# Optimization experiments

Measured on AMD Instinct MI355X. Metric: run time of the kernel, lower is better.

Reference implementation:

```python
import jax, jax.numpy as jnp
import numpy as np

N_TOKENS = 8192
D_MODEL = 1024
N_EXPERTS = 8
TOP_K = 2


def setup_inputs() -> dict:
    key = jax.random.key(0)
    ks = jax.random.split(key, 4)
    scale = 1.0 / np.sqrt(D_MODEL)
    x = jax.random.normal(ks[0], (N_TOKENS, D_MODEL), dtype=jnp.float32)
    gate_w = jax.random.uniform(ks[1], (N_EXPERTS, D_MODEL), jnp.float32, -scale, scale)
    expert_w = jax.random.uniform(ks[2], (N_EXPERTS, D_MODEL, D_MODEL), jnp.float32, -scale, scale)
    expert_b = jax.random.uniform(ks[3], (N_EXPERTS, D_MODEL), jnp.float32, -scale, scale)
    return {"x": x, "gate_w": gate_w, "expert_w": expert_w, "expert_b": expert_b}


def reference(x, gate_w, expert_w, expert_b):
    # Router: logits [N, E], softmax in fp32, top-k, renormalize over selected.
    router_logits = jnp.einsum('nd,ed->ne', x, gate_w)
    probs = jax.nn.softmax(router_logits.astype(jnp.float32), axis=1)
    rw, sel = jax.lax.top_k(probs, TOP_K)            # [N, K]
    rw = rw / jnp.sum(rw, axis=-1, keepdims=True)

    # Dense combine weights [N, E]: routing weight for selected experts, 0 else.
    n_idx = jnp.arange(x.shape[0])[:, None]
    w_dense = jnp.zeros((x.shape[0], N_EXPERTS), jnp.float32).at[n_idx, sel].set(rw)

    # Compute all experts for all tokens (vectorized equivalent of the
    # gather -> Linear -> weighted scatter-add loop; zero weight for
    # unselected experts reproduces the sparse dispatch exactly).
    # expert_w[e] is torch nn.Linear weight [out, in]: y = x @ W^T + b
    h = jnp.einsum('nd,ehd->neh', x, expert_w) + expert_b[None, :, :]  # [N, E, H]
    final = jnp.einsum('neh,ne->nh', h, w_dense.astype(x.dtype))
    return final, router_logits
```

## Files before the change

kernel.cpp:

```cpp
#include <hip/hip_runtime.h>
#include <hip/hip_bf16.h>
#include <stdint.h>

#define NT 8192
#define DM 1024
#define NE 8
#define MAX_TILES 160
#define SLOTS_MAX 17408
#define NKT (DM / 64)

typedef __bf16 bf16x8 __attribute__((ext_vector_type(8)));
typedef float f32x4 __attribute__((ext_vector_type(4)));

typedef const __attribute__((address_space(1))) void* gp_t;
typedef __attribute__((address_space(3))) void* lp_t;
#define GLDS(g, l) __builtin_amdgcn_global_load_lds((gp_t)(g), (lp_t)(l), 16, 0, 0)

__device__ inline unsigned short f2bf(float f) {
  unsigned int u = __float_as_uint(f);
  unsigned int r = (u + 0x7fffu + ((u >> 16) & 1u)) >> 16;
  return (unsigned short)r;
}
__device__ inline float bf2f(unsigned short u) {
  return __uint_as_float((unsigned int)u << 16);
}

__global__ void router_kernel(const float* __restrict__ x,
                              const float* __restrict__ gw,
                              float* __restrict__ logits,
                              unsigned short* __restrict__ xb,
                              int* __restrict__ top2e,
                              float* __restrict__ top2w) {
  const int n = blockIdx.x;
  const int lane = threadIdx.x;
  const float* xr = x + (size_t)n * DM;
  float s[NE];
#pragma unroll
  for (int e = 0; e < NE; ++e) s[e] = 0.f;
  for (int c = lane; c < DM; c += 64) {
    float xv = xr[c];
    xb[(size_t)n * DM + c] = f2bf(xv);
#pragma unroll
    for (int e = 0; e < NE; ++e) s[e] += xv * gw[e * DM + c];
  }
#pragma unroll
  for (int e = 0; e < NE; ++e) {
#pragma unroll
    for (int off = 32; off > 0; off >>= 1) s[e] += __shfl_xor(s[e], off);
  }
  if (lane == 0) {
    float m = s[0];
#pragma unroll
    for (int e = 1; e < NE; ++e) m = fmaxf(m, s[e]);
    float p[NE];
#pragma unroll
    for (int e = 0; e < NE; ++e) {
      p[e] = __expf(s[e] - m);
      logits[(size_t)n * NE + e] = s[e];
    }
    int e1 = 0; float b1 = p[0];
#pragma unroll
    for (int e = 1; e < NE; ++e) if (p[e] > b1) { b1 = p[e]; e1 = e; }
    int e2 = -1; float b2 = -1.f;
#pragma unroll
    for (int e = 0; e < NE; ++e) if (e != e1 && p[e] > b2) { b2 = p[e]; e2 = e; }
    float inv = 1.f / (b1 + b2);
    top2e[n * 2 + 0] = e1; top2e[n * 2 + 1] = e2;
    top2w[n * 2 + 0] = b1 * inv; top2w[n * 2 + 1] = b2 * inv;
  }
}

__global__ void cvt_w_kernel(const float* __restrict__ src,
                             unsigned short* __restrict__ dst) {
  size_t i = ((size_t)blockIdx.x * blockDim.x + threadIdx.x) * 8;
  float4 a = *(const float4*)(src + i);
  float4 b = *(const float4*)(src + i + 4);
  union { unsigned short u[8]; uint4 v; } o;
  o.u[0] = f2bf(a.x); o.u[1] = f2bf(a.y); o.u[2] = f2bf(a.z); o.u[3] = f2bf(a.w);
  o.u[4] = f2bf(b.x); o.u[5] = f2bf(b.y); o.u[6] = f2bf(b.z); o.u[7] = f2bf(b.w);
  *(uint4*)(dst + i) = o.v;
}

__global__ void count_kernel(const int* __restrict__ top2e, int* __restrict__ counts) {
  __shared__ int lcnt[NE];
  const int t = threadIdx.x;
  if (t < NE) lcnt[t] = 0;
  __syncthreads();
  const int n = blockIdx.x * 256 + t;
  atomicAdd(&lcnt[top2e[n * 2 + 0]], 1);
  atomicAdd(&lcnt[top2e[n * 2 + 1]], 1);
  __syncthreads();
  if (t < NE) atomicAdd(&counts[t], lcnt[t]);
}

__global__ void plan_kernel(const int* __restrict__ counts, int* __restrict__ seg_base,
                            int* __restrict__ tile_e, int* __restrict__ tile_row,
                            int* __restrict__ n_tiles) {
  __shared__ int sb[NE + 1], tb[NE + 1];
  const int lane = threadIdx.x;
  if (lane == 0) {
    int base = 0, tt = 0;
    for (int e = 0; e < NE; ++e) {
      sb[e] = base; tb[e] = tt;
      int c = counts[e];
      int nt = (c + 127) >> 7;
      tt += nt;
      base += nt << 7;
    }
    sb[NE] = base; tb[NE] = tt;
    *n_tiles = tt;
  }
  __syncthreads();
  if (lane <= NE) seg_base[lane] = sb[lane];
  const int total = tb[NE];
  for (int i = lane; i < total; i += 64) {
    int e = 0;
#pragma unroll
    for (int q = 0; q < NE; ++q) if (i >= tb[q + 1]) e = q + 1;
    tile_e[i] = e;
    tile_row[i] = sb[e] + (i - tb[e]) * 128;
  }
}

__global__ void scatter_kernel(const int* __restrict__ top2e,
                               const int* __restrict__ seg_base, int* __restrict__ counts2,
                               int* __restrict__ slot_token, int* __restrict__ tok2slot) {
  __shared__ int lcnt[NE], lbase[NE];
  const int t = threadIdx.x;
  if (t < NE) lcnt[t] = 0;
  __syncthreads();
  const int n = blockIdx.x * 256 + t;
  const int e0 = top2e[n * 2 + 0], e1 = top2e[n * 2 + 1];
  const int p0 = atomicAdd(&lcnt[e0], 1);
  const int p1 = atomicAdd(&lcnt[e1], 1);
  __syncthreads();
  if (t < NE) lbase[t] = seg_base[t] + atomicAdd(&counts2[t], lcnt[t]);
  __syncthreads();
  const int q0 = lbase[e0] + p0, q1 = lbase[e1] + p1;
  slot_token[q0] = n; slot_token[q1] = n;
  tok2slot[n * 2 + 0] = q0;
  tok2slot[n * 2 + 1] = q1;
}

__global__ __launch_bounds__(256, 2) void moe_gemm_kernel(
    const unsigned short* __restrict__ xb,
    const unsigned short* __restrict__ wb,
    const float* __restrict__ bias,
    const int* __restrict__ slot_token,
    const int* __restrict__ tile_e, const int* __restrict__ tile_row,
    const int* __restrict__ n_tiles,
    unsigned short* __restrict__ y)
{
  const int bm = blockIdx.x >> 3;
  const int bn = blockIdx.x & 7;
  if (bm >= *n_tiles) return;
  const int e = tile_e[bm];
  const int row0 = tile_row[bm];
  const int n0 = bn * 128;

  __shared__ __align__(16) unsigned short lA[2][8192];
  __shared__ __align__(16) unsigned short lB[2][8192];

  const int t = threadIdx.x;
  const int lane = t & 63;
  const int w = t >> 6;
  const int wm = w >> 1, wn = w & 1;

  const int srow = t >> 3;
  const int ss = (t & 7) ^ (srow & 7);
  const unsigned short* asrc[4];
  const unsigned short* bsrc[4];
#pragma unroll
  for (int c = 0; c < 4; ++c) {
    const int lr = c * 32 + srow;
    const int tok = slot_token[row0 + lr];
    asrc[c] = xb + (size_t)tok * DM + ss * 8;
    bsrc[c] = wb + (size_t)e * DM * DM + (size_t)(n0 + lr) * DM + ss * 8;
  }

  f32x4 acc[4][4];
#pragma unroll
  for (int i = 0; i < 4; ++i)
#pragma unroll
    for (int j = 0; j < 4; ++j) acc[i][j] = (f32x4){0.f, 0.f, 0.f, 0.f};

  auto stage = [&](int buf, int kt) {
    const int ko = kt * 64;
#pragma unroll
    for (int c = 0; c < 4; ++c) {
      GLDS(asrc[c] + ko, &lA[buf][c * 2048 + w * 512]);
      GLDS(bsrc[c] + ko, &lB[buf][c * 2048 + w * 512]);
    }
  };

  stage(0, 0);
  stage(1, 1);

  for (int kt = 0; kt < NKT; ++kt) {
    if (kt < NKT - 1) {
      asm volatile("s_waitcnt vmcnt(8)" ::: "memory");
    } else {
      asm volatile("s_waitcnt vmcnt(0)" ::: "memory");
    }
    __builtin_amdgcn_sched_barrier(0);
    __builtin_amdgcn_s_barrier();

    const int cur = kt & 1;
    bf16x8 af[2][4], bf[2][4];
#pragma unroll
    for (int ks = 0; ks < 2; ++ks) {
      const int kb = ks * 64 + (lane >> 4) * 16;
#pragma unroll
      for (int mi = 0; mi < 4; ++mi) {
        const int row = wm * 64 + mi * 16 + (lane & 15);
        af[ks][mi] = *(const bf16x8*)((const char*)lA[cur] + row * 128 + (kb ^ ((row & 7) << 4)));
      }
#pragma unroll
      for (int ni = 0; ni < 4; ++ni) {
        const int row = wn * 64 + ni * 16 + (lane & 15);
        bf[ks][ni] = *(const bf16x8*)((const char*)lB[cur] + row * 128 + (kb ^ ((row & 7) << 4)));
      }
    }
    __builtin_amdgcn_s_setprio(1);
#pragma unroll
    for (int ks = 0; ks < 2; ++ks)
#pragma unroll
      for (int mi = 0; mi < 4; ++mi)
#pragma unroll
        for (int ni = 0; ni < 4; ++ni)
          acc[mi][ni] = __builtin_amdgcn_mfma_f32_16x16x32_bf16(af[ks][mi], bf[ks][ni], acc[mi][ni], 0, 0, 0);
    __builtin_amdgcn_s_setprio(0);

    __builtin_amdgcn_sched_barrier(0);
    __builtin_amdgcn_s_barrier();
    if (kt + 2 < NKT) stage(cur, kt + 2);
  }

  const int cgrp = lane >> 4, ccol = lane & 15;
  float bv[4];
#pragma unroll
  for (int ni = 0; ni < 4; ++ni)
    bv[ni] = bias[e * DM + n0 + wn * 64 + ni * 16 + ccol];
#pragma unroll
  for (int mi = 0; mi < 4; ++mi) {
#pragma unroll
    for (int j = 0; j < 4; ++j) {
      const int r = row0 + wm * 64 + mi * 16 + cgrp * 4 + j;
      unsigned short* yrow = y + (size_t)r * DM + n0 + wn * 64;
#pragma unroll
      for (int ni = 0; ni < 4; ++ni)
        yrow[ni * 16 + ccol] = f2bf(acc[mi][ni][j] + bv[ni]);
    }
  }
}

__global__ void combine_kernel(const unsigned short* __restrict__ y,
                               const int* __restrict__ tok2slot,
                               const float* __restrict__ top2w,
                               float* __restrict__ out) {
  const int n = blockIdx.x;
  const int c = threadIdx.x;
  const int s0 = tok2slot[n * 2 + 0], s1 = tok2slot[n * 2 + 1];
  const float w0 = top2w[n * 2 + 0], w1 = top2w[n * 2 + 1];
  ushort4 a = *(const ushort4*)(y + (size_t)s0 * DM + c * 4);
  ushort4 b = *(const ushort4*)(y + (size_t)s1 * DM + c * 4);
  float4 r;
  r.x = w0 * bf2f(a.x) + w1 * bf2f(b.x);
  r.y = w0 * bf2f(a.y) + w1 * bf2f(b.y);
  r.z = w0 * bf2f(a.z) + w1 * bf2f(b.z);
  r.w = w0 * bf2f(a.w) + w1 * bf2f(b.w);
  *(float4*)(out + (size_t)n * DM + c * 4) = r;
}

extern "C" void kernel_launch(void* const* d_in, const int* in_sizes, int n_in,
                              void* d_out, int out_size, void* d_ws, size_t ws_size,
                              hipStream_t stream) {
  const float* x  = (const float*)d_in[0];
  const float* gw = (const float*)d_in[1];
  const float* ew = (const float*)d_in[2];
  const float* eb = (const float*)d_in[3];
  float* out    = (float*)d_out;
  float* logits = out + (size_t)NT * DM;

  char* ws = (char*)d_ws;
  int*   counts     = (int*)(ws + 0);
  int*   counts2    = (int*)(ws + 64);
  int*   seg_base   = (int*)(ws + 128);
  int*   n_tiles    = (int*)(ws + 192);
  int*   tile_e     = (int*)(ws + 256);
  int*   tile_row   = (int*)(ws + 1024);
  int*   top2e      = (int*)(ws + 2048);
  float* top2w      = (float*)(ws + 67584);
  int*   slot_token = (int*)(ws + 133120);
  int*   tok2slot   = (int*)(ws + 202752);
  unsigned short* xb = (unsigned short*)(ws + 272384);
  unsigned short* wb = (unsigned short*)(ws + 272384 + 16777216);
  unsigned short* y  = (unsigned short*)(ws + 272384 + 2 * 16777216);

  hipMemsetAsync(ws, 0, 256, stream);
  hipMemsetAsync(slot_token, 0, (size_t)SLOTS_MAX * 4, stream);

  cvt_w_kernel<<<(NE * DM * DM) / 8 / 256, 256, 0, stream>>>(ew, wb);
  router_kernel<<<NT, 64, 0, stream>>>(x, gw, logits, xb, top2e, top2w);
  count_kernel<<<NT / 256, 256, 0, stream>>>(top2e, counts);
  plan_kernel<<<1, 64, 0, stream>>>(counts, seg_base, tile_e, tile_row, n_tiles);
  scatter_kernel<<<NT / 256, 256, 0, stream>>>(top2e, seg_base, counts2, slot_token, tok2slot);
  moe_gemm_kernel<<<MAX_TILES * 8, 256, 0, stream>>>(xb, wb, eb, slot_token,
                                                     tile_e, tile_row, n_tiles, y);
  combine_kernel<<<NT, 256, 0, stream>>>(y, tok2slot, top2w, out);
}
```

Baseline: 111.8 us.

## Halve GEMM K-tile to raise occupancy and swizzle block order by column

Cuts the MoE GEMM K step from 64 to 32, which halves the LDS footprint (16KB per buffer pair) and raises launch bounds to 4 blocks per SIMD-group. The LDS row layout is repacked with a new XOR swizzle so that two 32-wide rows share one 128-byte line. Block IDs are remapped so consecutive blocks share the same N column tile across M tiles, aiming for better L2 reuse of expert weights. In exchange there are twice as many barrier/wait iterations with half the MFMA work per barrier, which could expose more latency.

Result: no change. 112.0 us (+0.2%).

```diff
diff --git a/kernel.cpp b/kernel.cpp
--- a/kernel.cpp
+++ b/kernel.cpp
@@ -7,7 +7,7 @@
 #define NE 8
 #define MAX_TILES 160
 #define SLOTS_MAX 17408
-#define NKT (DM / 64)
+#define NKT 32
 
 typedef __bf16 bf16x8 __attribute__((ext_vector_type(8)));
 typedef float f32x4 __attribute__((ext_vector_type(4)));
@@ -142,7 +142,7 @@
   tok2slot[n * 2 + 1] = q1;
 }
 
-__global__ __launch_bounds__(256, 2) void moe_gemm_kernel(
+__global__ __launch_bounds__(256, 4) void moe_gemm_kernel(
     const unsigned short* __restrict__ xb,
     const unsigned short* __restrict__ wb,
     const float* __restrict__ bias,
@@ -151,31 +151,32 @@
     const int* __restrict__ n_tiles,
     unsigned short* __restrict__ y)
 {
-  const int bm = blockIdx.x >> 3;
-  const int bn = blockIdx.x & 7;
+  const int bid = blockIdx.x;
+  const int swz = (bid & 7) * 160 + (bid >> 3);
+  const int bm = swz >> 3;
+  const int bn = swz & 7;
   if (bm >= *n_tiles) return;
   const int e = tile_e[bm];
   const int row0 = tile_row[bm];
   const int n0 = bn * 128;
 
-  __shared__ __align__(16) unsigned short lA[2][8192];
-  __shared__ __align__(16) unsigned short lB[2][8192];
+  __shared__ __align__(16) unsigned short lA[2][4096];
+  __shared__ __align__(16) unsigned short lB[2][4096];
 
   const int t = threadIdx.x;
   const int lane = t & 63;
   const int w = t >> 6;
   const int wm = w >> 1, wn = w & 1;
 
-  const int srow = t >> 3;
-  const int ss = (t & 7) ^ (srow & 7);
-  const unsigned short* asrc[4];
-  const unsigned short* bsrc[4];
-#pragma unroll
-  for (int c = 0; c < 4; ++c) {
-    const int lr = c * 32 + srow;
+  const int sS = (t & 7) ^ ((t >> 3) & 7);
+  const unsigned short* asrc[2];
+  const unsigned short* bsrc[2];
+#pragma unroll
+  for (int c = 0; c < 2; ++c) {
+    const int lr = c * 64 + ((t >> 3) << 1) + (sS >> 2);
     const int tok = slot_token[row0 + lr];
-    asrc[c] = xb + (size_t)tok * DM + ss * 8;
-    bsrc[c] = wb + (size_t)e * DM * DM + (size_t)(n0 + lr) * DM + ss * 8;
+    asrc[c] = xb + (size_t)tok * DM + (sS & 3) * 8;
+    bsrc[c] = wb + (size_t)e * DM * DM + (size_t)(n0 + lr) * DM + (sS & 3) * 8;
   }
 
   f32x4 acc[4][4];
@@ -185,20 +186,21 @@
     for (int j = 0; j < 4; ++j) acc[i][j] = (f32x4){0.f, 0.f, 0.f, 0.f};
 
   auto stage = [&](int buf, int kt) {
-    const int ko = kt * 64;
-#pragma unroll
-    for (int c = 0; c < 4; ++c) {
-      GLDS(asrc[c] + ko, &lA[buf][c * 2048 + w * 512]);
-      GLDS(bsrc[c] + ko, &lB[buf][c * 2048 + w * 512]);
+    const int ko = kt * 32;
+#pragma unroll
+    for (int c = 0; c < 2; ++c) {
+      GLDS(asrc[c] + ko, &lA[buf][c * 2048 + t * 8]);
+      GLDS(bsrc[c] + ko, &lB[buf][c * 2048 + t * 8]);
     }
   };
 
   stage(0, 0);
   stage(1, 1);
 
+  const int q = lane >> 4;
   for (int kt = 0; kt < NKT; ++kt) {
     if (kt < NKT - 1) {
-      asm volatile("s_waitcnt vmcnt(8)" ::: "memory");
+      asm volatile("s_waitcnt vmcnt(4)" ::: "memory");
     } else {
       asm volatile("s_waitcnt vmcnt(0)" ::: "memory");
     }
@@ -206,29 +208,25 @@
     __builtin_amdgcn_s_barrier();
 
     const int cur = kt & 1;
-    bf16x8 af[2][4], bf[2][4];
-#pragma unroll
-    for (int ks = 0; ks < 2; ++ks) {
-      const int kb = ks * 64 + (lane >> 4) * 16;
-#pragma unroll
-      for (int mi = 0; mi < 4; ++mi) {
-        const int row = wm * 64 + mi * 16 + (lane & 15);
-        af[ks][mi] = *(const bf16x8*)((const char*)lA[cur] + row * 128 + (kb ^ ((row & 7) << 4)));
-      }
-#pragma unroll
-      for (int ni = 0; ni < 4; ++ni) {
-        const int row = wn * 64 + ni * 16 + (lane & 15);
-        bf[ks][ni] = *(const bf16x8*)((const char*)lB[cur] + row * 128 + (kb ^ ((row & 7) << 4)));
-      }
+    bf16x8 af[4], bf[4];
+#pragma unroll
+    for (int mi = 0; mi < 4; ++mi) {
+      const int row = wm * 64 + mi * 16 + (lane & 15);
+      const int off = (row >> 1) * 128 + (((((row & 1) << 2) | q) ^ ((row >> 1) & 7)) << 4);
+      af[mi] = *(const bf16x8*)((const char*)lA[cur] + off);
+    }
+#pragma unroll
+    for (int ni = 0; ni < 4; ++ni) {
+      const int row = wn * 64 + ni * 16 + (lane & 15);
+      const int off = (row >> 1) * 128 + (((((row & 1) << 2) | q) ^ ((row >> 1) & 7)) << 4);
+      bf[ni] = *(const bf16x8*)((const char*)lB[cur] + off);
     }
     __builtin_amdgcn_s_setprio(1);
 #pragma unroll
-    for (int ks = 0; ks < 2; ++ks)
-#pragma unroll
-      for (int mi = 0; mi < 4; ++mi)
-#pragma unroll
-        for (int ni = 0; ni < 4; ++ni)
-          acc[mi][ni] = __builtin_amdgcn_mfma_f32_16x16x32_bf16(af[ks][mi], bf[ks][ni], acc[mi][ni], 0, 0, 0);
+    for (int mi = 0; mi < 4; ++mi)
+#pragma unroll
+      for (int ni = 0; ni < 4; ++ni)
+        acc[mi][ni] = __builtin_amdgcn_mfma_f32_16x16x32_bf16(af[mi], bf[ni], acc[mi][ni], 0, 0, 0);
     __builtin_amdgcn_s_setprio(0);
 
     __builtin_amdgcn_sched_barrier(0);
```

## Fuse weight conversion with router into one launch and swizzle GEMM block order

Applied to the files above, without the earlier changes.

The fp32-to-bf16 expert-weight conversion and the router are merged into a single prep kernel. The first 4096 blocks convert weights and the remaining blocks run the router with four tokens per 256-thread block instead of one token per 64-thread block. This removes a launch and lets the two independent jobs share the GPU at the same time. The MoE GEMM also remaps its block index so consecutive blocks walk M tiles with a fixed N tile, and early-exiting empty tiles are spread across the grid. That remap may change L2 reuse of expert weights versus activations, for better or worse.

Measured after the change: 105.1 us. 1.06x faster.

```diff
diff --git a/kernel.cpp b/kernel.cpp
--- a/kernel.cpp
+++ b/kernel.cpp
@@ -25,14 +25,24 @@
   return __uint_as_float((unsigned int)u << 16);
 }
 
-__global__ void router_kernel(const float* __restrict__ x,
-                              const float* __restrict__ gw,
-                              float* __restrict__ logits,
-                              unsigned short* __restrict__ xb,
-                              int* __restrict__ top2e,
-                              float* __restrict__ top2w) {
-  const int n = blockIdx.x;
-  const int lane = threadIdx.x;
+__global__ void prep_kernel(const float* __restrict__ ew, unsigned short* __restrict__ wb,
+                            const float* __restrict__ x, const float* __restrict__ gw,
+                            float* __restrict__ logits, unsigned short* __restrict__ xb,
+                            int* __restrict__ top2e, float* __restrict__ top2w) {
+  const int b = blockIdx.x;
+  const int t = threadIdx.x;
+  if (b < 4096) {
+    size_t i = ((size_t)b * 256 + t) * 8;
+    float4 a = *(const float4*)(ew + i);
+    float4 c = *(const float4*)(ew + i + 4);
+    union { unsigned short u[8]; uint4 v; } o;
+    o.u[0] = f2bf(a.x); o.u[1] = f2bf(a.y); o.u[2] = f2bf(a.z); o.u[3] = f2bf(a.w);
+    o.u[4] = f2bf(c.x); o.u[5] = f2bf(c.y); o.u[6] = f2bf(c.z); o.u[7] = f2bf(c.w);
+    *(uint4*)(wb + i) = o.v;
+    return;
+  }
+  const int lane = t & 63;
+  const int n = (b - 4096) * 4 + (t >> 6);
   const float* xr = x + (size_t)n * DM;
   float s[NE];
 #pragma unroll
@@ -68,17 +78,6 @@
     top2e[n * 2 + 0] = e1; top2e[n * 2 + 1] = e2;
     top2w[n * 2 + 0] = b1 * inv; top2w[n * 2 + 1] = b2 * inv;
   }
-}
-
-__global__ void cvt_w_kernel(const float* __restrict__ src,
-                             unsigned short* __restrict__ dst) {
-  size_t i = ((size_t)blockIdx.x * blockDim.x + threadIdx.x) * 8;
-  float4 a = *(const float4*)(src + i);
-  float4 b = *(const float4*)(src + i + 4);
-  union { unsigned short u[8]; uint4 v; } o;
-  o.u[0] = f2bf(a.x); o.u[1] = f2bf(a.y); o.u[2] = f2bf(a.z); o.u[3] = f2bf(a.w);
-  o.u[4] = f2bf(b.x); o.u[5] = f2bf(b.y); o.u[6] = f2bf(b.z); o.u[7] = f2bf(b.w);
-  *(uint4*)(dst + i) = o.v;
 }
 
 __global__ void count_kernel(const int* __restrict__ top2e, int* __restrict__ counts) {
@@ -151,8 +150,10 @@
     const int* __restrict__ n_tiles,
     unsigned short* __restrict__ y)
 {
-  const int bm = blockIdx.x >> 3;
-  const int bn = blockIdx.x & 7;
+  const int bid = blockIdx.x;
+  const int swz = (bid & 7) * 160 + (bid >> 3);
+  const int bm = swz >> 3;
+  const int bn = swz & 7;
   if (bm >= *n_tiles) return;
   const int e = tile_e[bm];
   const int row0 = tile_row[bm];
@@ -300,8 +301,7 @@
   hipMemsetAsync(ws, 0, 256, stream);
   hipMemsetAsync(slot_token, 0, (size_t)SLOTS_MAX * 4, stream);
 
-  cvt_w_kernel<<<(NE * DM * DM) / 8 / 256, 256, 0, stream>>>(ew, wb);
-  router_kernel<<<NT, 64, 0, stream>>>(x, gw, logits, xb, top2e, top2w);
+  prep_kernel<<<4096 + NT / 4, 256, 0, stream>>>(ew, wb, x, gw, logits, xb, top2e, top2w);
   count_kernel<<<NT / 256, 256, 0, stream>>>(top2e, counts);
   plan_kernel<<<1, 64, 0, stream>>>(counts, seg_base, tile_e, tile_row, n_tiles);
   scatter_kernel<<<NT / 256, 256, 0, stream>>>(top2e, seg_base, counts2, slot_token, tok2slot);
```
